# Performance work log

Hardware: AMD Instinct MI355X
Metric: run time of the kernel (lower is better)

Reference implementation:

```python
import jax, jax.numpy as jnp
import numpy as np

FACTOR = 2  # StyleGAN upsample factor
K1D = jnp.array([1.0, 4.0, 6.0, 4.0, 1.0], dtype=jnp.float32)
# StyleGAN upfirdn padding for upsample: p = kw - factor = 3
# pad0 = (p+1)//2 + factor - 1 = 3 ; pad1 = p//2 = 1 (+1 extra trailing zero
# because lhs_dilation gives length 2D-1 while zero-insertion gives 2D)
PAD0, PAD1 = 3, 2


def _upfir_axis(x, k1d, axis):
    """Zero-insert (factor 2) + 5-tap FIR along one spatial axis, depthwise.

    x: [N, C, D, H, W]; axis in {2, 3, 4}.
    """
    C = x.shape[1]
    kshape = [1, 1, 1]
    kshape[axis - 2] = k1d.shape[0]
    kernel = jnp.broadcast_to(k1d.reshape(kshape), (C, 1) + tuple(kshape))
    dil = [1, 1, 1]
    dil[axis - 2] = FACTOR
    pad = [(0, 0)] * 3
    pad[axis - 2] = (PAD0, PAD1)
    return jax.lax.conv_general_dilated(
        x, kernel.astype(x.dtype),
        window_strides=(1, 1, 1), padding=pad, lhs_dilation=dil,
        dimension_numbers=('NCDHW', 'OIDHW', 'NCDHW'),
        feature_group_count=C)


def setup_inputs() -> dict:
    key = jax.random.key(0)
    x = jax.random.normal(key, (4, 32, 48, 48, 48), dtype=jnp.float32)
    return {"x": x}


def reference(x):
    # normalize so kernel sums to 1, then apply gain factor per axis so the
    # total gain is factor**3 (StyleGAN: k = k/sum(k) * gain * factor**ndim,
    # split evenly across the 3 separable passes -> factor per axis)
    k = (K1D / K1D.sum() * FACTOR).astype(x.dtype)
    for ax in (2, 3, 4):  # D, H, W
        x = _upfir_axis(x, k, ax)
    return x  # [N, C, 2D, 2H, 2W]
```

## Files before the change

kernel.cpp:

```cpp
#include <hip/hip_runtime.h>


#define IN_D 48
#define IN_H 48
#define IN_W 48
#define NC   128
#define TD   8
#define TH   16
#define TW   16
#define LZ   (TD + 2)
#define LY   (TH + 2)
#define LX   (TW + 2)
#define LXP  (LX + 1)

__global__ __launch_bounds__(TW * TH)
void upfir3d_kernel(const float* __restrict__ in,
                    float* __restrict__ out) {
    __shared__ float lds[LZ * LY * LXP];

    const int tx = threadIdx.x;
    const int ty = threadIdx.y;
    const int bw = blockIdx.x;
    const int bh = blockIdx.y;
    const int bz = blockIdx.z;
    const int dz = bz % (IN_D / TD);
    const int nc = bz / (IN_D / TD);

    const int iw0 = bw * TW;
    const int ih0 = bh * TH;
    const int id0 = dz * TD;
    const size_t in_base = (size_t)nc * (IN_D * IN_H * IN_W);

    const int tid = ty * TW + tx;
    for (int idx = tid; idx < LZ * LY * LX; idx += TW * TH) {
        int z   = idx / (LY * LX);
        int rem = idx - z * (LY * LX);
        int y   = rem / LX;
        int xx  = rem - y * LX;
        int gd = id0 - 1 + z;
        int gh = ih0 - 1 + y;
        int gw = iw0 - 1 + xx;
        float v = 0.0f;
        if ((unsigned)gd < (unsigned)IN_D && (unsigned)gh < (unsigned)IN_H &&
            (unsigned)gw < (unsigned)IN_W) {
            v = in[in_base + ((size_t)gd * IN_H + gh) * IN_W + gw];
        }
        lds[(z * LY + y) * LXP + xx] = v;
    }
    __syncthreads();

    const int lx = tx + 1;
    const int ly = ty + 1;

    auto whpart = [&](int z) -> float4 {
        const float* p = &lds[(z * LY + (ly - 1)) * LXP + (lx - 1)];
        float rE[3], rO[3];
#pragma unroll
        for (int dy = 0; dy < 3; ++dy) {
            float v0 = p[dy * LXP + 0];
            float v1 = p[dy * LXP + 1];
            float v2 = p[dy * LXP + 2];
            rE[dy] = 0.5f * (v0 + v1);
            rO[dy] = 0.125f * (v0 + v2) + 0.75f * v1;
        }
        float4 q;
        q.x = 0.5f * (rE[0] + rE[1]);
        q.y = 0.5f * (rO[0] + rO[1]);
        q.z = 0.125f * (rE[0] + rE[2]) + 0.75f * rE[1];
        q.w = 0.125f * (rO[0] + rO[2]) + 0.75f * rO[1];
        return q;
    };

    float4 qm = whpart(0);
    float4 qc = whpart(1);

    const int OD = 2 * IN_D, OH = 2 * IN_H, OW = 2 * IN_W;
    const int ow = 2 * (iw0 + tx);
    const int oh = 2 * (ih0 + ty);
    float* obase = out + (size_t)nc * OD * OH * OW;

    auto store_rows = [&](int od_, float4 v) {
        size_t base = ((size_t)od_ * OH + oh) * OW + ow;
        float2 r0 = make_float2(v.x, v.y);
        float2 r1 = make_float2(v.z, v.w);
        *reinterpret_cast<float2*>(obase + base)      = r0;
        *reinterpret_cast<float2*>(obase + base + OW) = r1;
    };

#pragma unroll
    for (int d = 0; d < TD; ++d) {
        float4 qp = whpart(d + 2);
        int od = 2 * (id0 + d);

        float4 e, o;
        e.x = 0.5f * (qm.x + qc.x);
        e.y = 0.5f * (qm.y + qc.y);
        e.z = 0.5f * (qm.z + qc.z);
        e.w = 0.5f * (qm.w + qc.w);
        o.x = 0.125f * (qm.x + qp.x) + 0.75f * qc.x;
        o.y = 0.125f * (qm.y + qp.y) + 0.75f * qc.y;
        o.z = 0.125f * (qm.z + qp.z) + 0.75f * qc.z;
        o.w = 0.125f * (qm.w + qp.w) + 0.75f * qc.w;

        store_rows(od,     e);
        store_rows(od + 1, o);

        qm = qc;
        qc = qp;
    }
}

extern "C" void kernel_launch(void* const* d_in, const int* in_sizes, int n_in,
                              void* d_out, int out_size, void* d_ws, size_t ws_size,
                              hipStream_t stream) {
    const float* x = (const float*)d_in[0];
    float* out = (float*)d_out;

    dim3 grid(IN_W / TW, IN_H / TH, (IN_D / TD) * NC);
    dim3 block(TW, TH, 1);
    upfir3d_kernel<<<grid, block, 0, stream>>>(x, out);
}
```

Measured before the change: 489.0 us.

## Process two input columns per thread over full-width tiles with float4 stores

Each thread now computes two adjacent input columns, producing four output columns, and writes them with float4 stores instead of float2. Tiles now cover the full W extent, which removes horizontal halo reloads and shares LDS reads between neighbouring columns. The trade-off is a larger LDS footprint per block and fewer threads per block, which may reduce occupancy.

```diff
diff --git a/kernel.cpp b/kernel.cpp
--- a/kernel.cpp
+++ b/kernel.cpp
@@ -7,39 +7,50 @@
 #define NC   128
 #define TD   8
 #define TH   16
-#define TW   16
-#define LZ   (TD + 2)
-#define LY   (TH + 2)
-#define LX   (TW + 2)
-#define LXP  (LX + 1)
+#define NTX  24
+#define NTHREADS (NTX * TH)
+#define LZ (TD + 2)
+#define LY (TH + 2)
+#define LX (IN_W + 2)
+#define LXP (LX + 1)
 
-__global__ __launch_bounds__(TW * TH)
+__device__ __forceinline__ float4 f4_even(float4 a, float4 b) {
+    return make_float4(0.5f * (a.x + b.x), 0.5f * (a.y + b.y),
+                       0.5f * (a.z + b.z), 0.5f * (a.w + b.w));
+}
+__device__ __forceinline__ float4 f4_odd(float4 a, float4 b, float4 c) {
+    return make_float4(0.125f * (a.x + c.x) + 0.75f * b.x,
+                       0.125f * (a.y + c.y) + 0.75f * b.y,
+                       0.125f * (a.z + c.z) + 0.75f * b.z,
+                       0.125f * (a.w + c.w) + 0.75f * b.w);
+}
+
+struct Q { float4 E, O; };
+
+__global__ __launch_bounds__(NTHREADS)
 void upfir3d_kernel(const float* __restrict__ in,
                     float* __restrict__ out) {
     __shared__ float lds[LZ * LY * LXP];
 
     const int tx = threadIdx.x;
     const int ty = threadIdx.y;
-    const int bw = blockIdx.x;
-    const int bh = blockIdx.y;
-    const int bz = blockIdx.z;
-    const int dz = bz % (IN_D / TD);
-    const int nc = bz / (IN_D / TD);
+    const int bh = blockIdx.x;
+    const int dz = blockIdx.y;
+    const int nc = blockIdx.z;
 
-    const int iw0 = bw * TW;
     const int ih0 = bh * TH;
     const int id0 = dz * TD;
     const size_t in_base = (size_t)nc * (IN_D * IN_H * IN_W);
 
-    const int tid = ty * TW + tx;
-    for (int idx = tid; idx < LZ * LY * LX; idx += TW * TH) {
+    const int tid = ty * NTX + tx;
+    for (int idx = tid; idx < LZ * LY * LX; idx += NTHREADS) {
         int z   = idx / (LY * LX);
         int rem = idx - z * (LY * LX);
         int y   = rem / LX;
         int xx  = rem - y * LX;
         int gd = id0 - 1 + z;
         int gh = ih0 - 1 + y;
-        int gw = iw0 - 1 + xx;
+        int gw = xx - 1;
         float v = 0.0f;
         if ((unsigned)gd < (unsigned)IN_D && (unsigned)gh < (unsigned)IN_H &&
             (unsigned)gw < (unsigned)IN_W) {
@@ -49,61 +60,49 @@
     }
     __syncthreads();
 
-    const int lx = tx + 1;
     const int ly = ty + 1;
+    const int c0 = 2 * tx;
 
-    auto whpart = [&](int z) -> float4 {
-        const float* p = &lds[(z * LY + (ly - 1)) * LXP + (lx - 1)];
-        float rE[3], rO[3];
+    auto whpart = [&](int z) -> Q {
+        const float* p = &lds[(z * LY + (ly - 1)) * LXP + c0];
+        float4 r[3];
 #pragma unroll
         for (int dy = 0; dy < 3; ++dy) {
             float v0 = p[dy * LXP + 0];
             float v1 = p[dy * LXP + 1];
             float v2 = p[dy * LXP + 2];
-            rE[dy] = 0.5f * (v0 + v1);
-            rO[dy] = 0.125f * (v0 + v2) + 0.75f * v1;
+            float v3 = p[dy * LXP + 3];
+            r[dy].x = 0.5f * (v0 + v1);
+            r[dy].y = 0.125f * (v0 + v2) + 0.75f * v1;
+            r[dy].z = 0.5f * (v1 + v2);
+            r[dy].w = 0.125f * (v1 + v3) + 0.75f * v2;
         }
-        float4 q;
-        q.x = 0.5f * (rE[0] + rE[1]);
-        q.y = 0.5f * (rO[0] + rO[1]);
-        q.z = 0.125f * (rE[0] + rE[2]) + 0.75f * rE[1];
-        q.w = 0.125f * (rO[0] + rO[2]) + 0.75f * rO[1];
+        Q q;
+        q.E = f4_even(r[0], r[1]);
+        q.O = f4_odd(r[0], r[1], r[2]);
         return q;
     };
 
-    float4 qm = whpart(0);
-    float4 qc = whpart(1);
+    Q qm = whpart(0);
+    Q qc = whpart(1);
 
     const int OD = 2 * IN_D, OH = 2 * IN_H, OW = 2 * IN_W;
-    const int ow = 2 * (iw0 + tx);
+    const int ow = 4 * tx;
     const int oh = 2 * (ih0 + ty);
-    float* obase = out + (size_t)nc * OD * OH * OW;
-
-    auto store_rows = [&](int od_, float4 v) {
-        size_t base = ((size_t)od_ * OH + oh) * OW + ow;
-        float2 r0 = make_float2(v.x, v.y);
-        float2 r1 = make_float2(v.z, v.w);
-        *reinterpret_cast<float2*>(obase + base)      = r0;
-        *reinterpret_cast<float2*>(obase + base + OW) = r1;
-    };
+    float* ob = out + (size_t)nc * OD * OH * OW;
 
 #pragma unroll
     for (int d = 0; d < TD; ++d) {
-        float4 qp = whpart(d + 2);
-        int od = 2 * (id0 + d);
+        Q qp = whpart(d + 2);
+        const int od = 2 * (id0 + d);
 
-        float4 e, o;
-        e.x = 0.5f * (qm.x + qc.x);
-        e.y = 0.5f * (qm.y + qc.y);
-        e.z = 0.5f * (qm.z + qc.z);
-        e.w = 0.5f * (qm.w + qc.w);
-        o.x = 0.125f * (qm.x + qp.x) + 0.75f * qc.x;
-        o.y = 0.125f * (qm.y + qp.y) + 0.75f * qc.y;
-        o.z = 0.125f * (qm.z + qp.z) + 0.75f * qc.z;
-        o.w = 0.125f * (qm.w + qp.w) + 0.75f * qc.w;
+        size_t b0 = ((size_t)od * OH + oh) * OW + ow;
+        *reinterpret_cast<float4*>(ob + b0)      = f4_even(qm.E, qc.E);
+        *reinterpret_cast<float4*>(ob + b0 + OW) = f4_even(qm.O, qc.O);
 
-        store_rows(od,     e);
-        store_rows(od + 1, o);
+        size_t b1 = b0 + (size_t)OH * OW;
+        *reinterpret_cast<float4*>(ob + b1)      = f4_odd(qm.E, qc.E, qp.E);
+        *reinterpret_cast<float4*>(ob + b1 + OW) = f4_odd(qm.O, qc.O, qp.O);
 
         qm = qc;
         qc = qp;
@@ -116,7 +115,7 @@
     const float* x = (const float*)d_in[0];
     float* out = (float*)d_out;
 
-    dim3 grid(IN_W / TW, IN_H / TH, (IN_D / TD) * NC);
-    dim3 block(TW, TH, 1);
+    dim3 grid(IN_H / TH, IN_D / TD, NC);
+    dim3 block(NTX, TH, 1);
     upfir3d_kernel<<<grid, block, 0, stream>>>(x, out);
 }
```

New measurement: 519.1 us. 6.2% more time.
